# Kernel tuning notes

Measured on AMD Instinct MI355X. Metric: run time of the kernel, lower is better.

The kernel has to match this reference:

```python
import jax, jax.numpy as jnp
import numpy as np
import math

N_HEAD = 16
ROPE_BASE = 10000.0


def _rope_as_in_source(x):
    """Faithful replication of RotaryPositionalEmbeddings.forward applied to
    x of shape [B, H, T, hd] (called after transpose in the source, so
    seq_len = x.size(1) = H: angles are indexed by head index, not position)."""
    B, H, T, hd = x.shape
    theta = 1.0 / (ROPE_BASE ** (jnp.arange(0, hd, 2, dtype=jnp.float32) / hd))  # [hd/2]
    ang = jnp.arange(H, dtype=jnp.float32)[:, None] * theta[None, :]  # [H, hd/2]
    cos = jnp.cos(ang)[None, :, None, :]  # [1, H, 1, hd/2]
    sin = jnp.sin(ang)[None, :, None, :]
    xr = x.reshape(B, H, T, hd // 2, 2)
    out = jnp.stack([
        xr[..., 0] * cos - xr[..., 1] * sin,
        xr[..., 1] * cos + xr[..., 0] * sin,
    ], axis=-1)
    return out.reshape(B, H, T, hd)


def setup_inputs() -> dict:
    key = jax.random.key(0)
    ks = jax.random.split(key, 5)
    B, T, C = 2, 2048, 1024
    s = 0.02
    return {
        "x": jax.random.normal(ks[0], (B, T, C), dtype=jnp.float32),
        "W_attn": jax.random.normal(ks[1], (C, 3 * C), dtype=jnp.float32) * s,
        "b_attn": jnp.zeros((3 * C,), dtype=jnp.float32),
        "W_proj": jax.random.normal(ks[2], (C, C), dtype=jnp.float32) * s,
        "b_proj": jnp.zeros((C,), dtype=jnp.float32),
    }


def reference(x, W_attn, b_attn, W_proj, b_proj):
    B, T, C = x.shape
    H = N_HEAD
    hd = C // H
    qkv = x @ W_attn + b_attn  # [B, T, 3C]
    q, k, v = jnp.split(qkv, 3, axis=2)
    # [B, T, H, hd] -> [B, H, T, hd]
    q = q.reshape(B, T, H, hd).transpose(0, 2, 1, 3)
    k = k.reshape(B, T, H, hd).transpose(0, 2, 1, 3)
    v = v.reshape(B, T, H, hd).transpose(0, 2, 1, 3)
    q = _rope_as_in_source(q)
    k = _rope_as_in_source(k)
    att = jnp.einsum("bhqd,bhkd->bhqk", q, k) * (1.0 / math.sqrt(hd))
    causal = jnp.tril(jnp.ones((T, T), dtype=bool))
    att = jnp.where(causal[None, None, :, :], att, -jnp.inf)
    att = jax.nn.softmax(att, axis=-1)
    y = jnp.einsum("bhqk,bhkd->bhqd", att, v)  # [B, H, T, hd]
    y = y.transpose(0, 2, 1, 3).reshape(B, T, C)
    return y @ W_proj + b_proj
```

## Files before the change

### kernel.cpp

```cpp
#include <hip/hip_runtime.h>

typedef __attribute__((ext_vector_type(8))) short bf16x8;
typedef __attribute__((ext_vector_type(4))) float f32x4;
typedef __attribute__((ext_vector_type(4))) unsigned int uint4v;
typedef unsigned short ushort_t;

#define BB 2
#define TT 2048
#define CC 1024
#define HH 16
#define HD 64
#define MM (BB * TT)
#define N3C (3 * CC)

__device__ __forceinline__ ushort_t f2b(float f) {
  unsigned u = __builtin_bit_cast(unsigned, f);
  u += 0x7fffu + ((u >> 16) & 1u);
  return (ushort_t)(u >> 16);
}

__device__ __forceinline__ unsigned pack2bf(float a, float b) {
  unsigned ua = (__builtin_bit_cast(unsigned, a) + 0x8000u) >> 16;
  unsigned ub = (__builtin_bit_cast(unsigned, b) + 0x8000u) & 0xffff0000u;
  return ua | ub;
}

__device__ __forceinline__ float fexp2(float x) {
#if __has_builtin(__builtin_amdgcn_exp2f)
  return __builtin_amdgcn_exp2f(x);
#else
  return __expf(x * 0.6931471805599453f);
#endif
}

__device__ __forceinline__ f32x4 mfma16(bf16x8 a, bf16x8 b, f32x4 c) {
  return __builtin_amdgcn_mfma_f32_16x16x32_bf16(a, b, c, 0, 0, 0);
}

__device__ __forceinline__ void load_lds16(const void* g, void* l) {
  __builtin_amdgcn_global_load_lds((const __attribute__((address_space(1))) void*)g,
                                   (__attribute__((address_space(3))) void*)l, 16, 0, 0);
}

__global__ __launch_bounds__(256) void cast_f32_bf16(const float* __restrict__ x,
                                                     ushort_t* __restrict__ o, int n4) {
  int i = blockIdx.x * 256 + threadIdx.x;
  if (i >= n4) return;
  const float4 v = ((const float4*)x)[i];
  typedef __attribute__((ext_vector_type(4))) ushort_t us4;
  us4 r;
  r.x = f2b(v.x); r.y = f2b(v.y); r.z = f2b(v.z); r.w = f2b(v.w);
  ((us4*)o)[i] = r;
}

__global__ __launch_bounds__(256) void transpose_cast(const float* __restrict__ W,
                                                      ushort_t* __restrict__ Wt,
                                                      int R, int Nc) {
  __shared__ ushort_t tile[32][33];
  int n0 = blockIdx.x * 32, r0 = blockIdx.y * 32;
  int c = threadIdx.x, rr = threadIdx.y;
#pragma unroll
  for (int i = 0; i < 4; ++i) {
    int r = rr + i * 8;
    tile[r][c] = f2b(W[(size_t)(r0 + r) * Nc + n0 + c]);
  }
  __syncthreads();
#pragma unroll
  for (int i = 0; i < 4; ++i) {
    int r = rr + i * 8;
    Wt[(size_t)(n0 + r) * R + r0 + c] = tile[c][r];
  }
}

template <int EPI>
__global__ __launch_bounds__(256) void gemm_bt(const ushort_t* __restrict__ A,
                                               const ushort_t* __restrict__ Bt,
                                               const float* __restrict__ bias,
                                               ushort_t* __restrict__ qo,
                                               ushort_t* __restrict__ ko,
                                               ushort_t* __restrict__ vto,
                                               float* __restrict__ outp,
                                               int N, int K) {
  __shared__ __align__(16) ushort_t As[128 * 32];
  __shared__ __align__(16) ushort_t Bs[128 * 32];
  const int tid = threadIdx.x, lane = tid & 63, wave = tid >> 6;
  const int l15 = lane & 15, quad = lane >> 4;
  const int wm = (wave >> 1) * 64, wn = (wave & 1) * 64;
  const int m0 = blockIdx.y * 128, n0 = blockIdx.x * 128;

  f32x4 acc[4][4] = {};
  for (int k0 = 0; k0 < K; k0 += 32) {
    __syncthreads();
#pragma unroll
    for (int p = 0; p < 2; ++p) {
      int e = (p * 256 + tid) * 8;
      int r = e >> 5, c = e & 31;
      load_lds16(&A[(size_t)(m0 + r) * K + k0 + c], &As[e]);
      load_lds16(&Bt[(size_t)(n0 + r) * K + k0 + c], &Bs[e]);
    }
    __syncthreads();
    bf16x8 af[4], bfr[4];
#pragma unroll
    for (int i = 0; i < 4; ++i) {
      af[i]  = *(const bf16x8*)&As[(wm + i * 16 + l15) * 32 + quad * 8];
      bfr[i] = *(const bf16x8*)&Bs[(wn + i * 16 + l15) * 32 + quad * 8];
    }
#pragma unroll
    for (int i = 0; i < 4; ++i)
#pragma unroll
      for (int j = 0; j < 4; ++j)
        acc[i][j] = mfma16(af[i], bfr[j], acc[i][j]);
  }

#pragma unroll
  for (int i = 0; i < 4; ++i) {
#pragma unroll
    for (int j = 0; j < 4; ++j) {
#pragma unroll
      for (int r = 0; r < 4; ++r) {
        int gr = m0 + wm + i * 16 + quad * 4 + r;
        int gc = n0 + wn + j * 16 + l15;
        float v = acc[i][j][r] + bias[gc];
        if (EPI == 0) {
          int sec = gc >> 10, cc = gc & 1023, h = cc >> 6, d = cc & 63;
          int b = gr >> 11, t = gr & 2047;
          int bh = b * HH + h;
          ushort_t hv = f2b(v);
          if (sec == 0) {
            int si = t >> 4, lq = t & 15, dh = d >> 5, qd = (d >> 3) & 3, j8 = d & 7;
            qo[((((size_t)bh * 128 + si) * 2 + dh) * 64 + qd * 16 + lq) * 8 + j8] = hv;
          } else if (sec == 1) {
            int kbi = t >> 6, ng = (t >> 4) & 3, lk = t & 15;
            int dh = d >> 5, qd = (d >> 3) & 3, j8 = d & 7;
            ko[((((size_t)bh * 32 + kbi) * 8 + ng * 2 + dh) * 64 + qd * 16 + lk) * 8 + j8] = hv;
          } else {
            int kbi = t >> 6, kk = t & 63;
            int h_ = kk >> 5, jh = (kk >> 4) & 1, qd = (kk >> 2) & 3, j8 = jh * 4 + (kk & 3);
            int dg = d >> 4, lv = d & 15;
            vto[((((size_t)bh * 32 + kbi) * 8 + dg * 2 + h_) * 64 + qd * 16 + lv) * 8 + j8] = hv;
          }
        } else {
          outp[(size_t)gr * N + gc] = v;
        }
      }
    }
  }
}

__global__ __launch_bounds__(256) void attn_kernel(const ushort_t* __restrict__ Qf,
                                                   const ushort_t* __restrict__ Kf,
                                                   const ushort_t* __restrict__ Vf,
                                                   ushort_t* __restrict__ y) {
  __shared__ __align__(16) float red[2][2176];
  const int tid = threadIdx.x, lane = tid & 63, wave = tid >> 6;
  const int l15 = lane & 15, quad = lane >> 4;
  const int idx = blockIdx.x;
  const int xcd = idx & 7, j = idx >> 3;
  const int bh = xcd * 4 + (j & 3);
  const int g = 63 - (j >> 2);
  const int qs = g * 32;
  const int nk = (qs + 95) >> 6;

  const float SCL = 0.125f * 1.4426950408889634f;

  const ushort_t* qbase = Qf + (((size_t)bh * 128 + (qs >> 4)) * 2 * 64 + lane) * 8;
  bf16x8 qf[2][2];
#pragma unroll
  for (int st = 0; st < 2; ++st)
#pragma unroll
    for (int dh = 0; dh < 2; ++dh)
      qf[st][dh] = *(const bf16x8*)(qbase + (st * 2 + dh) * 512);

  f32x4 o[2][4] = {};
  float l_r[2] = {0.f, 0.f};

  for (int it = wave; it < nk; it += 4) {
    const bool diag = (it == nk - 1);
    const size_t tb = ((size_t)bh * 32 + it) * 4096 + (size_t)lane * 8;
    bf16x8 kf[4][2], vf[4][2];
#pragma unroll
    for (int ng = 0; ng < 4; ++ng)
#pragma unroll
      for (int dh = 0; dh < 2; ++dh)
        kf[ng][dh] = *(const bf16x8*)(Kf + tb + (ng * 2 + dh) * 512);
#pragma unroll
    for (int dg = 0; dg < 4; ++dg)
#pragma unroll
      for (int h = 0; h < 2; ++h)
        vf[dg][h] = *(const bf16x8*)(Vf + tb + (dg * 2 + h) * 512);

#pragma unroll
    for (int st = 0; st < 2; ++st) {
      f32x4 s[4];
#pragma unroll
      for (int ng = 0; ng < 4; ++ng) {
        f32x4 z = {};
        z = mfma16(kf[ng][0], qf[st][0], z);
        z = mfma16(kf[ng][1], qf[st][1], z);
        s[ng] = z;
      }
      float p[4][4];
      const int qg = qs + st * 16 + l15;
#pragma unroll
      for (int ng = 0; ng < 4; ++ng)
#pragma unroll
        for (int r = 0; r < 4; ++r) {
          float pv = fexp2(s[ng][r] * SCL);
          if (diag) {
            int kg = it * 64 + ng * 16 + quad * 4 + r;
            pv = (kg > qg) ? 0.f : pv;
          }
          p[ng][r] = pv;
          l_r[st] += pv;
        }
      union { uint4v u; bf16x8 v; } pk0, pk1;
      pk0.u[0] = pack2bf(p[0][0], p[0][1]); pk0.u[1] = pack2bf(p[0][2], p[0][3]);
      pk0.u[2] = pack2bf(p[1][0], p[1][1]); pk0.u[3] = pack2bf(p[1][2], p[1][3]);
      pk1.u[0] = pack2bf(p[2][0], p[2][1]); pk1.u[1] = pack2bf(p[2][2], p[2][3]);
      pk1.u[2] = pack2bf(p[3][0], p[3][1]); pk1.u[3] = pack2bf(p[3][2], p[3][3]);
#pragma unroll
      for (int dg = 0; dg < 4; ++dg) {
        o[st][dg] = mfma16(vf[dg][0], pk0.v, o[st][dg]);
        o[st][dg] = mfma16(vf[dg][1], pk1.v, o[st][dg]);
      }
    }
  }

  auto dump = [&](float* buf) {
#pragma unroll
    for (int st = 0; st < 2; ++st)
#pragma unroll
      for (int dg = 0; dg < 4; ++dg)
        *(f32x4*)&buf[(st * 4 + dg) * 256 + lane * 4] = o[st][dg];
    buf[2048 + lane * 2 + 0] = l_r[0];
    buf[2048 + lane * 2 + 1] = l_r[1];
  };
  auto merge = [&](const float* buf) {
#pragma unroll
    for (int st = 0; st < 2; ++st)
#pragma unroll
      for (int dg = 0; dg < 4; ++dg)
        o[st][dg] += *(const f32x4*)&buf[(st * 4 + dg) * 256 + lane * 4];
    l_r[0] += buf[2048 + lane * 2 + 0];
    l_r[1] += buf[2048 + lane * 2 + 1];
  };
  if (wave == 1) dump(red[0]);
  if (wave == 3) dump(red[1]);
  __syncthreads();
  if (wave == 0) merge(red[0]);
  if (wave == 2) merge(red[1]);
  __syncthreads();
  if (wave == 2) dump(red[0]);
  __syncthreads();
  if (wave == 0) {
    merge(red[0]);
    const int b = bh >> 4, h = bh & 15;
#pragma unroll
    for (int st = 0; st < 2; ++st) {
      float lf = l_r[st];
      lf += __shfl_xor(lf, 16);
      lf += __shfl_xor(lf, 32);
      const float inv = 1.0f / lf;
      const size_t row = (size_t)(b * TT + qs + st * 16 + l15) * CC;
#pragma unroll
      for (int dg = 0; dg < 4; ++dg) {
        uint2 u;
        u.x = (unsigned)f2b(o[st][dg][0] * inv) | ((unsigned)f2b(o[st][dg][1] * inv) << 16);
        u.y = (unsigned)f2b(o[st][dg][2] * inv) | ((unsigned)f2b(o[st][dg][3] * inv) << 16);
        *(uint2*)&y[row + h * HD + dg * 16 + quad * 4] = u;
      }
    }
  }
}

extern "C" void kernel_launch(void* const* d_in, const int* in_sizes, int n_in,
                              void* d_out, int out_size, void* d_ws, size_t ws_size,
                              hipStream_t stream) {
  const float* x  = (const float*)d_in[0];
  const float* Wa = (const float*)d_in[1];
  const float* ba = (const float*)d_in[2];
  const float* Wp = (const float*)d_in[3];
  const float* bp = (const float*)d_in[4];
  float* out = (float*)d_out;

  char* ws = (char*)d_ws;
  ushort_t* xb  = (ushort_t*)(ws + 0);
  ushort_t* wat = (ushort_t*)(ws + 8388608);
  ushort_t* wpt = (ushort_t*)(ws + 14680064);
  ushort_t* Qf  = (ushort_t*)(ws + 16777216);
  ushort_t* Kf  = (ushort_t*)(ws + 25165824);
  ushort_t* Vf  = (ushort_t*)(ws + 33554432);
  ushort_t* yb  = (ushort_t*)(ws + 41943040);

  cast_f32_bf16<<<(MM * CC / 4 + 255) / 256, 256, 0, stream>>>(x, xb, MM * CC / 4);
  transpose_cast<<<dim3(N3C / 32, CC / 32), dim3(32, 8), 0, stream>>>(Wa, wat, CC, N3C);
  transpose_cast<<<dim3(CC / 32, CC / 32), dim3(32, 8), 0, stream>>>(Wp, wpt, CC, CC);

  gemm_bt<0><<<dim3(N3C / 128, MM / 128), 256, 0, stream>>>(
      xb, wat, ba, Qf, Kf, Vf, nullptr, N3C, CC);

  attn_kernel<<<2048, 256, 0, stream>>>(Qf, Kf, Vf, yb);

  gemm_bt<1><<<dim3(CC / 128, MM / 128), 256, 0, stream>>>(
      yb, wpt, bp, nullptr, nullptr, nullptr, out, CC, CC);
}
```

Measured before the change: 190.2 us.

## Fuse prep kernels, deepen GEMM K-tile, simplify QKV epilogue, narrow proj tile

Merges the x cast and the two weight transpose-casts into one prep launch to cut launch overhead. The GEMM now stages a K-depth of 64 per barrier pair, as two 32-wide panels, halving the number of sync rounds. The QKV epilogue's per-element index math is replaced by precomputed base pointers, with vectorized stores for V. The output projection uses 128x64 tiles to double its block count and fill more CUs. LDS use per block grows and the epilogue layout assumptions are now hardcoded.

```diff
diff --git a/kernel.cpp b/kernel.cpp
--- a/kernel.cpp
+++ b/kernel.cpp
@@ -19,6 +19,10 @@
   return (ushort_t)(u >> 16);
 }
 
+__device__ __forceinline__ unsigned pack2rne(float a, float b) {
+  return (unsigned)f2b(a) | ((unsigned)f2b(b) << 16);
+}
+
 __device__ __forceinline__ unsigned pack2bf(float a, float b) {
   unsigned ua = (__builtin_bit_cast(unsigned, a) + 0x8000u) >> 16;
   unsigned ub = (__builtin_bit_cast(unsigned, b) + 0x8000u) & 0xffff0000u;
@@ -42,23 +46,34 @@
                                    (__attribute__((address_space(3))) void*)l, 16, 0, 0);
 }
 
-__global__ __launch_bounds__(256) void cast_f32_bf16(const float* __restrict__ x,
-                                                     ushort_t* __restrict__ o, int n4) {
-  int i = blockIdx.x * 256 + threadIdx.x;
-  if (i >= n4) return;
-  const float4 v = ((const float4*)x)[i];
-  typedef __attribute__((ext_vector_type(4))) ushort_t us4;
-  us4 r;
-  r.x = f2b(v.x); r.y = f2b(v.y); r.z = f2b(v.z); r.w = f2b(v.w);
-  ((us4*)o)[i] = r;
-}
-
-__global__ __launch_bounds__(256) void transpose_cast(const float* __restrict__ W,
-                                                      ushort_t* __restrict__ Wt,
-                                                      int R, int Nc) {
+__global__ __launch_bounds__(256) void prep(const float* __restrict__ x,
+                                            const float* __restrict__ Wa,
+                                            const float* __restrict__ Wp,
+                                            ushort_t* __restrict__ xb,
+                                            ushort_t* __restrict__ wat,
+                                            ushort_t* __restrict__ wpt) {
+  const int blk = blockIdx.x, tid = threadIdx.x;
+  if (blk < 4096) {
+    int i = blk * 256 + tid;
+    const float4 v = ((const float4*)x)[i];
+    typedef __attribute__((ext_vector_type(4))) ushort_t us4;
+    us4 r;
+    r.x = f2b(v.x); r.y = f2b(v.y); r.z = f2b(v.z); r.w = f2b(v.w);
+    ((us4*)xb)[i] = r;
+    return;
+  }
   __shared__ ushort_t tile[32][33];
-  int n0 = blockIdx.x * 32, r0 = blockIdx.y * 32;
-  int c = threadIdx.x, rr = threadIdx.y;
+  const float* W; ushort_t* Wt; int R, Nc, n0, r0;
+  if (blk < 7168) {
+    int tb = blk - 4096;
+    W = Wa; Wt = wat; R = CC; Nc = N3C;
+    n0 = (tb % 96) * 32; r0 = (tb / 96) * 32;
+  } else {
+    int tb = blk - 7168;
+    W = Wp; Wt = wpt; R = CC; Nc = CC;
+    n0 = (tb & 31) * 32; r0 = (tb >> 5) * 32;
+  }
+  const int c = tid & 31, rr = tid >> 5;
 #pragma unroll
   for (int i = 0; i < 4; ++i) {
     int r = rr + i * 8;
@@ -72,7 +87,7 @@
   }
 }
 
-template <int EPI>
+template <int EPI, int NT>
 __global__ __launch_bounds__(256) void gemm_bt(const ushort_t* __restrict__ A,
                                                const ushort_t* __restrict__ Bt,
                                                const float* __restrict__ bias,
@@ -81,69 +96,91 @@
                                                ushort_t* __restrict__ vto,
                                                float* __restrict__ outp,
                                                int N, int K) {
-  __shared__ __align__(16) ushort_t As[128 * 32];
-  __shared__ __align__(16) ushort_t Bs[128 * 32];
+  constexpr int NJ = NT / 32;
+  __shared__ __align__(16) ushort_t As[128 * 64];
+  __shared__ __align__(16) ushort_t Bs[NT * 64];
   const int tid = threadIdx.x, lane = tid & 63, wave = tid >> 6;
   const int l15 = lane & 15, quad = lane >> 4;
-  const int wm = (wave >> 1) * 64, wn = (wave & 1) * 64;
-  const int m0 = blockIdx.y * 128, n0 = blockIdx.x * 128;
-
-  f32x4 acc[4][4] = {};
-  for (int k0 = 0; k0 < K; k0 += 32) {
+  const int wm = (wave >> 1) * 64, wn = (wave & 1) * (NT / 2);
+  const int m0 = blockIdx.y * 128, n0 = blockIdx.x * NT;
+
+  f32x4 acc[4][NJ] = {};
+  for (int k0 = 0; k0 < K; k0 += 64) {
     __syncthreads();
 #pragma unroll
-    for (int p = 0; p < 2; ++p) {
-      int e = (p * 256 + tid) * 8;
-      int r = e >> 5, c = e & 31;
-      load_lds16(&A[(size_t)(m0 + r) * K + k0 + c], &As[e]);
-      load_lds16(&Bt[(size_t)(n0 + r) * K + k0 + c], &Bs[e]);
+    for (int p = 0; p < 4; ++p) {
+      int d16 = p * 256 + tid;
+      int pan = d16 >> 9, rem = d16 & 511, row = rem >> 2, cc = rem & 3;
+      load_lds16(&A[(size_t)(m0 + row) * K + k0 + pan * 32 + cc * 8], &As[d16 * 8]);
+    }
+#pragma unroll
+    for (int p = 0; p < NT / 32; ++p) {
+      int d16 = p * 256 + tid;
+      int pan = d16 / (NT * 4), rem = d16 % (NT * 4), row = rem >> 2, cc = rem & 3;
+      load_lds16(&Bt[(size_t)(n0 + row) * K + k0 + pan * 32 + cc * 8], &Bs[d16 * 8]);
     }
     __syncthreads();
-    bf16x8 af[4], bfr[4];
-#pragma unroll
-    for (int i = 0; i < 4; ++i) {
-      af[i]  = *(const bf16x8*)&As[(wm + i * 16 + l15) * 32 + quad * 8];
-      bfr[i] = *(const bf16x8*)&Bs[(wn + i * 16 + l15) * 32 + quad * 8];
-    }
+#pragma unroll
+    for (int pan = 0; pan < 2; ++pan) {
+      const ushort_t* Ap = &As[pan * 4096];
+      const ushort_t* Bp = &Bs[pan * (NT * 32)];
+      bf16x8 af[4], bfr[NJ];
+#pragma unroll
+      for (int i = 0; i < 4; ++i)
+        af[i] = *(const bf16x8*)&Ap[(wm + i * 16 + l15) * 32 + quad * 8];
+#pragma unroll
+      for (int j = 0; j < NJ; ++j)
+        bfr[j] = *(const bf16x8*)&Bp[(wn + j * 16 + l15) * 32 + quad * 8];
+#pragma unroll
+      for (int i = 0; i < 4; ++i)
+#pragma unroll
+        for (int j = 0; j < NJ; ++j)
+          acc[i][j] = mfma16(af[i], bfr[j], acc[i][j]);
+    }
+  }
+
+  float bv[NJ];
+#pragma unroll
+  for (int j = 0; j < NJ; ++j) bv[j] = bias[n0 + wn + j * 16 + l15];
+
+  if (EPI == 0) {
+    const int h8 = l15 >> 3, j8l = l15 & 7;
+    const int t0 = (m0 + wm) & 2047, b = (m0 + wm) >> 11;
+    const int gsec = (n0 + wn) >> 10, h = ((n0 + wn) & 1023) >> 6;
+    const int bh = b * HH + h;
+    if (gsec < 2) {
+      ushort_t* dst = (gsec == 0 ? qo + ((size_t)bh * 128 + (t0 >> 4)) * 1024
+                                 : ko + ((size_t)bh * 32 + (t0 >> 6)) * 4096)
+                      + h8 * 128 + quad * 32 + j8l;
+#pragma unroll
+      for (int i = 0; i < 4; ++i)
+#pragma unroll
+        for (int j = 0; j < 4; ++j)
+#pragma unroll
+          for (int r = 0; r < 4; ++r)
+            dst[i * 1024 + (j >> 1) * 512 + (j & 1) * 256 + r * 8] =
+                f2b(acc[i][j][r] + bv[j]);
+    } else {
+      ushort_t* dst = vto + ((size_t)bh * 32 + (t0 >> 6)) * 4096 + quad * 128 + l15 * 8;
+#pragma unroll
+      for (int j = 0; j < 4; ++j)
+#pragma unroll
+        for (int i = 0; i < 4; ++i) {
+          uint2 u;
+          u.x = pack2rne(acc[i][j][0] + bv[j], acc[i][j][1] + bv[j]);
+          u.y = pack2rne(acc[i][j][2] + bv[j], acc[i][j][3] + bv[j]);
+          *(uint2*)&dst[j * 1024 + (i >> 1) * 512 + (i & 1) * 4] = u;
+        }
+    }
+  } else {
 #pragma unroll
     for (int i = 0; i < 4; ++i)
 #pragma unroll
-      for (int j = 0; j < 4; ++j)
-        acc[i][j] = mfma16(af[i], bfr[j], acc[i][j]);
-  }
-
-#pragma unroll
-  for (int i = 0; i < 4; ++i) {
-#pragma unroll
-    for (int j = 0; j < 4; ++j) {
-#pragma unroll
       for (int r = 0; r < 4; ++r) {
-        int gr = m0 + wm + i * 16 + quad * 4 + r;
-        int gc = n0 + wn + j * 16 + l15;
-        float v = acc[i][j][r] + bias[gc];
-        if (EPI == 0) {
-          int sec = gc >> 10, cc = gc & 1023, h = cc >> 6, d = cc & 63;
-          int b = gr >> 11, t = gr & 2047;
-          int bh = b * HH + h;
-          ushort_t hv = f2b(v);
-          if (sec == 0) {
-            int si = t >> 4, lq = t & 15, dh = d >> 5, qd = (d >> 3) & 3, j8 = d & 7;
-            qo[((((size_t)bh * 128 + si) * 2 + dh) * 64 + qd * 16 + lq) * 8 + j8] = hv;
-          } else if (sec == 1) {
-            int kbi = t >> 6, ng = (t >> 4) & 3, lk = t & 15;
-            int dh = d >> 5, qd = (d >> 3) & 3, j8 = d & 7;
-            ko[((((size_t)bh * 32 + kbi) * 8 + ng * 2 + dh) * 64 + qd * 16 + lk) * 8 + j8] = hv;
-          } else {
-            int kbi = t >> 6, kk = t & 63;
-            int h_ = kk >> 5, jh = (kk >> 4) & 1, qd = (kk >> 2) & 3, j8 = jh * 4 + (kk & 3);
-            int dg = d >> 4, lv = d & 15;
-            vto[((((size_t)bh * 32 + kbi) * 8 + dg * 2 + h_) * 64 + qd * 16 + lv) * 8 + j8] = hv;
-          }
-        } else {
-          outp[(size_t)gr * N + gc] = v;
-        }
+        float* rp = outp + (size_t)(m0 + wm + i * 16 + quad * 4 + r) * N + n0 + wn + l15;
+#pragma unroll
+        for (int j = 0; j < NJ; ++j) rp[j * 16] = acc[i][j][r] + bv[j];
       }
-    }
   }
 }
 
@@ -265,8 +302,8 @@
 #pragma unroll
       for (int dg = 0; dg < 4; ++dg) {
         uint2 u;
-        u.x = (unsigned)f2b(o[st][dg][0] * inv) | ((unsigned)f2b(o[st][dg][1] * inv) << 16);
-        u.y = (unsigned)f2b(o[st][dg][2] * inv) | ((unsigned)f2b(o[st][dg][3] * inv) << 16);
+        u.x = pack2rne(o[st][dg][0] * inv, o[st][dg][1] * inv);
+        u.y = pack2rne(o[st][dg][2] * inv, o[st][dg][3] * inv);
         *(uint2*)&y[row + h * HD + dg * 16 + quad * 4] = u;
       }
     }
@@ -292,15 +329,13 @@
   ushort_t* Vf  = (ushort_t*)(ws + 33554432);
   ushort_t* yb  = (ushort_t*)(ws + 41943040);
 
-  cast_f32_bf16<<<(MM * CC / 4 + 255) / 256, 256, 0, stream>>>(x, xb, MM * CC / 4);
-  transpose_cast<<<dim3(N3C / 32, CC / 32), dim3(32, 8), 0, stream>>>(Wa, wat, CC, N3C);
-  transpose_cast<<<dim3(CC / 32, CC / 32), dim3(32, 8), 0, stream>>>(Wp, wpt, CC, CC);
-
-  gemm_bt<0><<<dim3(N3C / 128, MM / 128), 256, 0, stream>>>(
+  prep<<<8192, 256, 0, stream>>>(x, Wa, Wp, xb, wat, wpt);
+
+  gemm_bt<0, 128><<<dim3(N3C / 128, MM / 128), 256, 0, stream>>>(
       xb, wat, ba, Qf, Kf, Vf, nullptr, N3C, CC);
 
   attn_kernel<<<2048, 256, 0, stream>>>(Qf, Kf, Vf, yb);
 
-  gemm_bt<1><<<dim3(CC / 128, MM / 128), 256, 0, stream>>>(
+  gemm_bt<1, 64><<<dim3(CC / 64, MM / 128), 256, 0, stream>>>(
       yb, wpt, bp, nullptr, nullptr, nullptr, out, CC, CC);
 }
```

After: 170.3 us. 1.12x faster.
